# Optimization experiments

Hardware: AMD Instinct MI355X
Metric: run time of the kernel (lower is better)

The kernel has to match this reference:

```python
import jax, jax.numpy as jnp
import numpy as np

N_HEADS = 16
EMBED = 1024
HEAD_SIZE = 64
BLOCK = 2048
BATCH = 2
SEQ = 2048


def setup_inputs() -> dict:
    key = jax.random.key(0)
    ks = jax.random.split(key, 6)
    scale_e = 1.0 / np.sqrt(EMBED)
    x = jax.random.normal(ks[0], (BATCH, SEQ, EMBED), dtype=jnp.float32)
    # per-head Q/K/V projections (bias=False in nanoGPT-style SelfAttentionHead), stacked over heads
    wq = jax.random.normal(ks[1], (N_HEADS, EMBED, HEAD_SIZE), dtype=jnp.float32) * scale_e
    wk = jax.random.normal(ks[2], (N_HEADS, EMBED, HEAD_SIZE), dtype=jnp.float32) * scale_e
    wv = jax.random.normal(ks[3], (N_HEADS, EMBED, HEAD_SIZE), dtype=jnp.float32) * scale_e
    # output projection nn.Linear(embedding_size, embedding_size): y = x @ W^T + b
    w_proj = jax.random.normal(ks[4], (EMBED, EMBED), dtype=jnp.float32) * scale_e
    b_proj = jax.random.normal(ks[5], (EMBED,), dtype=jnp.float32) * 0.01
    return {"x": x, "wq": wq, "wk": wk, "wv": wv, "w_proj": w_proj, "b_proj": b_proj}


def reference(x, wq, wk, wv, w_proj, b_proj):
    B, S, E = x.shape
    # project all heads at once: [B, H, S, D]
    q = jnp.einsum('bse,hed->bhsd', x, wq)
    k = jnp.einsum('bse,hed->bhsd', x, wk)
    v = jnp.einsum('bse,hed->bhsd', x, wv)
    scale = 1.0 / jnp.sqrt(jnp.asarray(HEAD_SIZE, dtype=x.dtype))
    scores = jnp.einsum('bhqd,bhkd->bhqk', q, k) * scale  # [B,H,S,S]
    causal = jnp.tril(jnp.ones((S, S), dtype=bool))
    scores = jnp.where(causal, scores, -jnp.inf)
    attn = jax.nn.softmax(scores, axis=-1)  # (attn dropout inactive in eval)
    out = jnp.einsum('bhqk,bhkd->bhqd', attn, v)  # [B,H,S,D]
    # concat heads along last dim -> [B, S, H*D] == [B, S, E]
    out = out.transpose(0, 2, 1, 3).reshape(B, S, E)
    # output projection (dropout inactive in eval)
    return out @ w_proj.T + b_proj
```

## Files before the change

### kernel.cpp

```cpp
#include <hip/hip_runtime.h>
#include <hip/hip_bf16.h>


typedef __attribute__((ext_vector_type(4))) float  f32x4;
typedef __attribute__((ext_vector_type(8))) short  bf16x8;

#define S_LEN 2048
#define EMB   1024
#define NH    16
#define HD    64

#define LDSW 72

#define QSCALE 0.18033688011112042f
#define EXP2C  17.312340490667562f

#if __has_builtin(__builtin_amdgcn_exp2f)
#define EXP2(x) __builtin_amdgcn_exp2f(x)
#else
#define EXP2(x) __exp2f(x)
#endif

__device__ __forceinline__ unsigned short f2bf(float f) {
    __hip_bfloat16 h = __float2bfloat16(f);
    return __builtin_bit_cast(unsigned short, h);
}
__device__ __forceinline__ unsigned int pk2bf(float a, float b) {
    unsigned int x = __builtin_bit_cast(unsigned int, a);
    unsigned int y = __builtin_bit_cast(unsigned int, b);
    x += 0x7FFFu + ((x >> 16) & 1u);
    y += 0x7FFFu + ((y >> 16) & 1u);
    return (x >> 16) | (y & 0xFFFF0000u);
}

__global__ __launch_bounds__(256) void prep(const float* __restrict__ x,
                                            const float* __restrict__ wq,
                                            const float* __restrict__ wk,
                                            const float* __restrict__ wv,
                                            const float* __restrict__ wproj,
                                            unsigned short* __restrict__ xb,
                                            unsigned short* __restrict__ wpb,
                                            unsigned short* __restrict__ wcat) {
    int blk = blockIdx.x;
    if (blk < 5120) {
        const float* in = (blk < 4096) ? x : wproj;
        unsigned short* out = (blk < 4096) ? xb : wpb;
        int bb = (blk < 4096) ? blk : blk - 4096;
        int i = (bb * 256 + threadIdx.x) * 4;
        float4 v = *(const float4*)(in + i);
        out[i + 0] = f2bf(v.x);
        out[i + 1] = f2bf(v.y);
        out[i + 2] = f2bf(v.z);
        out[i + 3] = f2bf(v.w);
    } else {
        int b2  = blk - 5120;
        int et  = b2 & 7;
        int h   = (b2 >> 3) & 15;
        int qkv = b2 >> 7;
        const float* w = (qkv == 0) ? wq : (qkv == 1) ? wk : wv;
        int t = threadIdx.x;
        int d = t & 63, es = t >> 6;
        int e0 = et * 128 + es * 32;

        unsigned short val[32];
        #pragma unroll
        for (int i = 0; i < 32; i++)
            val[i] = f2bf(w[(size_t)h * 65536 + (size_t)(e0 + i) * 64 + d]);

        size_t n = (size_t)qkv * 1024 + h * 64 + d;
        #pragma unroll
        for (int k = 0; k < 4; k++)
            *(uint4*)(wcat + n * 1024 + e0 + k * 8) = *(const uint4*)(val + k * 8);
    }
}

__device__ __forceinline__ void gemm_tile_core(const unsigned short* __restrict__ A,
                                               const unsigned short* __restrict__ Bt,
                                               int K, int m0, int n0,
                                               unsigned short* As, unsigned short* Bs,
                                               f32x4 acc[4][4]) {
    const int t    = threadIdx.x;
    const int wave = t >> 6, lane = t & 63;
    const int wm   = (wave >> 1) * 64, wn = (wave & 1) * 64;
    const int lr   = lane & 15, quad = lane >> 4;
    const int sr   = t >> 3;
    const int sc   = (t & 7) * 8;

    #pragma unroll
    for (int i = 0; i < 4; i++)
        #pragma unroll
        for (int j = 0; j < 4; j++) acc[i][j] = (f32x4)(0.0f);

    for (int k0 = 0; k0 < K; k0 += 64) {
        __syncthreads();
        #pragma unroll
        for (int p = 0; p < 4; ++p) {
            int r = p * 32 + sr;
            uint4 av = *(const uint4*)(A  + (size_t)(m0 + r) * K + k0 + sc);
            uint4 bv = *(const uint4*)(Bt + (size_t)(n0 + r) * K + k0 + sc);
            *(uint4*)(As + r * LDSW + sc) = av;
            *(uint4*)(Bs + r * LDSW + sc) = bv;
        }
        __syncthreads();
        #pragma unroll
        for (int kk = 0; kk < 64; kk += 32) {
            bf16x8 af[4], bfr[4];
            #pragma unroll
            for (int i = 0; i < 4; i++)
                af[i] = *(const bf16x8*)(As + (wm + i * 16 + lr) * LDSW + kk + quad * 8);
            #pragma unroll
            for (int j = 0; j < 4; j++)
                bfr[j] = *(const bf16x8*)(Bs + (wn + j * 16 + lr) * LDSW + kk + quad * 8);
            #pragma unroll
            for (int i = 0; i < 4; i++)
                #pragma unroll
                for (int j = 0; j < 4; j++)
                    acc[i][j] = __builtin_amdgcn_mfma_f32_16x16x32_bf16(af[i], bfr[j], acc[i][j], 0, 0, 0);
        }
    }
}

__global__ __launch_bounds__(256) void gemm_qkv(const unsigned short* __restrict__ xb,
                                                const unsigned short* __restrict__ wcat,
                                                unsigned short* __restrict__ qb,
                                                unsigned short* __restrict__ kb,
                                                unsigned short* __restrict__ vt) {
    __shared__ unsigned short Smem[2 * 128 * LDSW];
    unsigned short* As = Smem;
    unsigned short* Bs = Smem + 128 * LDSW;
    f32x4 acc[4][4];
    int m0 = blockIdx.x * 128, n0 = blockIdx.y * 128;
    gemm_tile_core(xb, wcat, EMB, m0, n0, As, Bs, acc);

    int t = threadIdx.x, wave = t >> 6, lane = t & 63;
    int wm = (wave >> 1) * 64, wn = (wave & 1) * 64, lr = lane & 15, quad = lane >> 4;
    int b  = m0 >> 11;
    int s0 = m0 & 2047;
    unsigned short* Tb = Smem;

    if (n0 < 2048) {
        bool isQ = (n0 < 1024);
        unsigned short* dst = isQ ? qb : kb;
        float sc = isQ ? QSCALE : 1.0f;
        __syncthreads();
        #pragma unroll
        for (int i = 0; i < 4; i++)
            #pragma unroll
            for (int j = 0; j < 4; j++)
                #pragma unroll
                for (int e = 0; e < 4; e++)
                    Tb[(wm + i * 16 + quad * 4 + e) * 136 + wn + j * 16 + lr] = f2bf(acc[i][j][e] * sc);
        __syncthreads();
        #pragma unroll
        for (int p = 0; p < 8; p++) {
            int r  = p * 16 + (t >> 4);
            int ch = (t & 15) * 8;
            int n  = n0 + ch;
            int h  = (n >> 6) & 15, d = ch & 63;
            *(uint4*)(dst + (((size_t)(b * NH + h)) * S_LEN + s0 + r) * HD + d) =
                *(const uint4*)(Tb + r * 136 + ch);
        }
    } else {
        __syncthreads();
        #pragma unroll
        for (int i = 0; i < 4; i++)
            #pragma unroll
            for (int j = 0; j < 4; j++)
                #pragma unroll
                for (int e = 0; e < 4; e++)
                    Tb[(wn + j * 16 + lr) * 136 + (wm + i * 16 + quad * 4 + e)] = f2bf(acc[i][j][e]);
        __syncthreads();
        #pragma unroll
        for (int p = 0; p < 8; p++) {
            int nl  = p * 16 + (t >> 4);
            int n   = n0 + nl;
            int h   = (n >> 6) & 15, d = n & 63;
            int col = (t & 15) * 8;
            *(uint4*)(vt + (((size_t)(b * NH + h)) * HD + d) * S_LEN + s0 + col) =
                *(const uint4*)(Tb + nl * 136 + col);
        }
    }
}

__global__ __launch_bounds__(256) void gemm_proj(const unsigned short* __restrict__ ao,
                                                 const unsigned short* __restrict__ wpb,
                                                 const float* __restrict__ bproj,
                                                 float* __restrict__ out) {
    __shared__ unsigned short Smem[2 * 128 * LDSW];
    f32x4 acc[4][4];
    int m0 = blockIdx.x * 128, n0 = blockIdx.y * 128;
    gemm_tile_core(ao, wpb, EMB, m0, n0, Smem, Smem + 128 * LDSW, acc);

    int t = threadIdx.x, wave = t >> 6, lane = t & 63;
    int wm = (wave >> 1) * 64, wn = (wave & 1) * 64, lr = lane & 15, quad = lane >> 4;
    #pragma unroll
    for (int i = 0; i < 4; i++)
        #pragma unroll
        for (int j = 0; j < 4; j++) {
            int n = n0 + wn + j * 16 + lr;
            float bias = bproj[n];
            #pragma unroll
            for (int e = 0; e < 4; e++) {
                int m = m0 + wm + i * 16 + quad * 4 + e;
                out[(size_t)m * EMB + n] = acc[i][j][e] + bias;
            }
        }
}

__global__ __launch_bounds__(256) void attn_mfma(const unsigned short* __restrict__ qb,
                                                 const unsigned short* __restrict__ kb,
                                                 const unsigned short* __restrict__ vtb,
                                                 unsigned short* __restrict__ ao) {
    __shared__ unsigned short Ks[64 * LDSW];
    __shared__ unsigned short Vs[64 * LDSW];
    __shared__ unsigned short Ps[64 * LDSW];

    int bIdx = blockIdx.x;
    int bh   = bIdx & 31;
    int sidx = bIdx >> 5;
    int g = sidx >> 3, s = sidx & 7;
    int slab = (g == 0) ? 31 - s : (g == 1) ? s : (g == 2) ? 23 - s : 8 + s;
    int b = bh >> 4, h = bh & 15;
    int t = threadIdx.x, wave = t >> 6, lane = t & 63;
    int c = lane & 15, quad = lane >> 4;

    const unsigned short* Q  = qb  + (size_t)bh * S_LEN * HD;
    const unsigned short* K  = kb  + (size_t)bh * S_LEN * HD;
    const unsigned short* Vt = vtb + (size_t)bh * HD * S_LEN;

    int r0 = slab * 64;
    int rw = r0 + wave * 16;

    bf16x8 Qf[2];
    #pragma unroll
    for (int ks = 0; ks < 2; ks++)
        Qf[ks] = *(const bf16x8*)(Q + (size_t)(rw + c) * HD + ks * 32 + quad * 8);

    f32x4 O[4];
    f32x4 lacc = (f32x4)(0.0f);
    #pragma unroll
    for (int dt = 0; dt < 4; dt++) O[dt] = (f32x4)(0.0f);

    const short oneb = (short)0x3F80;
    bf16x8 ones = {oneb, oneb, oneb, oneb, oneb, oneb, oneb, oneb};

    unsigned short* Pw = Ps + wave * 16 * LDSW;
    int sr = t >> 3, scg = (t & 7) * 8;

    int kend = r0 + 64;
    uint4 kpre0 = *(const uint4*)(K  + (size_t)sr * HD + scg);
    uint4 kpre1 = *(const uint4*)(K  + (size_t)(sr + 32) * HD + scg);
    uint4 vpre0 = *(const uint4*)(Vt + (size_t)sr * S_LEN + scg);
    uint4 vpre1 = *(const uint4*)(Vt + (size_t)(sr + 32) * S_LEN + scg);

    for (int j0 = 0; j0 < kend; j0 += 64) {
        __syncthreads();
        *(uint4*)(Ks + sr * LDSW + scg)        = kpre0;
        *(uint4*)(Ks + (sr + 32) * LDSW + scg) = kpre1;
        *(uint4*)(Vs + sr * LDSW + scg)        = vpre0;
        *(uint4*)(Vs + (sr + 32) * LDSW + scg) = vpre1;
        __syncthreads();
        if (j0 + 64 < kend) {
            kpre0 = *(const uint4*)(K  + (size_t)(j0 + 64 + sr) * HD + scg);
            kpre1 = *(const uint4*)(K  + (size_t)(j0 + 96 + sr) * HD + scg);
            vpre0 = *(const uint4*)(Vt + (size_t)sr * S_LEN + j0 + 64 + scg);
            vpre1 = *(const uint4*)(Vt + (size_t)(sr + 32) * S_LEN + j0 + 64 + scg);
        }

        f32x4 S4[4];
        #pragma unroll
        for (int kt = 0; kt < 4; kt++) S4[kt] = (f32x4)(0.0f);
        __builtin_amdgcn_s_setprio(1);
        #pragma unroll
        for (int ks = 0; ks < 2; ks++) {
            bf16x8 Kf[4];
            #pragma unroll
            for (int kt = 0; kt < 4; kt++)
                Kf[kt] = *(const bf16x8*)(Ks + (kt * 16 + c) * LDSW + ks * 32 + quad * 8);
            #pragma unroll
            for (int kt = 0; kt < 4; kt++)
                S4[kt] = __builtin_amdgcn_mfma_f32_16x16x32_bf16(Kf[kt], Qf[ks], S4[kt], 0, 0, 0);
        }
        __builtin_amdgcn_s_setprio(0);

        bool need_mask = (j0 + 63 > rw);
        #pragma unroll
        for (int kt = 0; kt < 4; kt++) {
            float p0 = EXP2(S4[kt][0] - EXP2C);
            float p1 = EXP2(S4[kt][1] - EXP2C);
            float p2 = EXP2(S4[kt][2] - EXP2C);
            float p3 = EXP2(S4[kt][3] - EXP2C);
            if (need_mask) {
                int key  = j0 + kt * 16 + quad * 4;
                int qrow = rw + c;
                if (key + 0 > qrow) p0 = 0.0f;
                if (key + 1 > qrow) p1 = 0.0f;
                if (key + 2 > qrow) p2 = 0.0f;
                if (key + 3 > qrow) p3 = 0.0f;
            }
            uint2 pk;
            pk.x = pk2bf(p0, p1);
            pk.y = pk2bf(p2, p3);
            *(uint2*)(Pw + c * LDSW + kt * 16 + quad * 4) = pk;
        }

        __builtin_amdgcn_s_setprio(1);
        #pragma unroll
        for (int ks = 0; ks < 2; ks++) {
            bf16x8 Af = *(const bf16x8*)(Pw + c * LDSW + ks * 32 + quad * 8);
            lacc = __builtin_amdgcn_mfma_f32_16x16x32_bf16(Af, ones, lacc, 0, 0, 0);
            #pragma unroll
            for (int dt = 0; dt < 4; dt++) {
                bf16x8 Vf = *(const bf16x8*)(Vs + (dt * 16 + c) * LDSW + ks * 32 + quad * 8);
                O[dt] = __builtin_amdgcn_mfma_f32_16x16x32_bf16(Af, Vf, O[dt], 0, 0, 0);
            }
        }
        __builtin_amdgcn_s_setprio(0);
    }

    float inv[4];
    #pragma unroll
    for (int e = 0; e < 4; e++) inv[e] = 1.0f / lacc[e];

    #pragma unroll
    for (int dt = 0; dt < 4; dt++)
        #pragma unroll
        for (int e = 0; e < 4; e++)
            Ps[(wave * 16 + quad * 4 + e) * LDSW + dt * 16 + c] = f2bf(O[dt][e] * inv[e]);
    __syncthreads();
    #pragma unroll
    for (int p = 0; p < 2; p++) {
        int r = p * 32 + sr;
        *(uint4*)(ao + ((size_t)(b * S_LEN + r0 + r)) * EMB + h * HD + scg) =
            *(const uint4*)(Ps + r * LDSW + scg);
    }
}

extern "C" void kernel_launch(void* const* d_in, const int* in_sizes, int n_in,
                              void* d_out, int out_size, void* d_ws, size_t ws_size,
                              hipStream_t stream) {
    const float* x     = (const float*)d_in[0];
    const float* wq    = (const float*)d_in[1];
    const float* wk    = (const float*)d_in[2];
    const float* wv    = (const float*)d_in[3];
    const float* wproj = (const float*)d_in[4];
    const float* bproj = (const float*)d_in[5];
    float* out = (float*)d_out;

    char* ws = (char*)d_ws;
    unsigned short* xb   = (unsigned short*)(ws + 0);
    unsigned short* wcat = (unsigned short*)(ws + 8388608);
    unsigned short* wpb  = (unsigned short*)(ws + 14680064);
    unsigned short* qb   = (unsigned short*)(ws + 16777216);
    unsigned short* kb   = (unsigned short*)(ws + 25165824);
    unsigned short* vt   = (unsigned short*)(ws + 33554432);
    unsigned short* ao   = (unsigned short*)(ws + 41943040);

    prep<<<5504, 256, 0, stream>>>(x, wq, wk, wv, wproj, xb, wpb, wcat);
    gemm_qkv<<<dim3(32, 24), 256, 0, stream>>>(xb, wcat, qb, kb, vt);
    attn_mfma<<<1024, 256, 0, stream>>>(qb, kb, vt, ao);
    gemm_proj<<<dim3(32, 8), 256, 0, stream>>>(ao, wpb, bproj, out);
}
```

Baseline: 181.2 us.

## Process 128 query rows per attention block with double-buffered K/V tiles

Each attention block now runs 8 waves over a 128-row query chunk, so every K/V tile loaded into LDS serves twice as many query rows. K/V tiles are double-buffered, which cuts the loop to one barrier per tile, and the block order is rebalanced for the causal workload. Waves whose rows lie entirely before a tile skip it, so some waves sit idle at the diagonal. The LDS row pitch drops from 72 to 68, which also changes the GEMM kernels' padding and leaves 16-byte LDS accesses only 8-byte aligned. The fixed exponent offset is removed, which risks overflow in exp2 if scores grow large.

```diff
diff --git a/kernel.cpp b/kernel.cpp
--- a/kernel.cpp
+++ b/kernel.cpp
@@ -10,10 +10,9 @@
 #define NH    16
 #define HD    64
 
-#define LDSW 72
+#define LDSW 68
 
 #define QSCALE 0.18033688011112042f
-#define EXP2C  17.312340490667562f
 
 #if __has_builtin(__builtin_amdgcn_exp2f)
 #define EXP2(x) __builtin_amdgcn_exp2f(x)
@@ -207,19 +206,18 @@
         }
 }
 
-__global__ __launch_bounds__(256) void attn_mfma(const unsigned short* __restrict__ qb,
+__global__ __launch_bounds__(512) void attn_mfma(const unsigned short* __restrict__ qb,
                                                  const unsigned short* __restrict__ kb,
                                                  const unsigned short* __restrict__ vtb,
                                                  unsigned short* __restrict__ ao) {
-    __shared__ unsigned short Ks[64 * LDSW];
-    __shared__ unsigned short Vs[64 * LDSW];
-    __shared__ unsigned short Ps[64 * LDSW];
+    __shared__ unsigned short Ks[2][64 * LDSW];
+    __shared__ unsigned short Vs[2][64 * LDSW];
+    __shared__ unsigned short Ps[128 * LDSW];
 
     int bIdx = blockIdx.x;
     int bh   = bIdx & 31;
-    int sidx = bIdx >> 5;
-    int g = sidx >> 3, s = sidx & 7;
-    int slab = (g == 0) ? 31 - s : (g == 1) ? s : (g == 2) ? 23 - s : 8 + s;
+    int grp  = bIdx >> 5;
+    int chunk = (grp < 8) ? (15 - grp) : (grp - 8);
     int b = bh >> 4, h = bh & 15;
     int t = threadIdx.x, wave = t >> 6, lane = t & 63;
     int c = lane & 15, quad = lane >> 4;
@@ -228,7 +226,7 @@
     const unsigned short* K  = kb  + (size_t)bh * S_LEN * HD;
     const unsigned short* Vt = vtb + (size_t)bh * HD * S_LEN;
 
-    int r0 = slab * 64;
+    int r0 = chunk * 128;
     int rw = r0 + wave * 16;
 
     bf16x8 Qf[2];
@@ -247,75 +245,82 @@
     unsigned short* Pw = Ps + wave * 16 * LDSW;
     int sr = t >> 3, scg = (t & 7) * 8;
 
-    int kend = r0 + 64;
-    uint4 kpre0 = *(const uint4*)(K  + (size_t)sr * HD + scg);
-    uint4 kpre1 = *(const uint4*)(K  + (size_t)(sr + 32) * HD + scg);
-    uint4 vpre0 = *(const uint4*)(Vt + (size_t)sr * S_LEN + scg);
-    uint4 vpre1 = *(const uint4*)(Vt + (size_t)(sr + 32) * S_LEN + scg);
-
-    for (int j0 = 0; j0 < kend; j0 += 64) {
-        __syncthreads();
-        *(uint4*)(Ks + sr * LDSW + scg)        = kpre0;
-        *(uint4*)(Ks + (sr + 32) * LDSW + scg) = kpre1;
-        *(uint4*)(Vs + sr * LDSW + scg)        = vpre0;
-        *(uint4*)(Vs + (sr + 32) * LDSW + scg) = vpre1;
-        __syncthreads();
-        if (j0 + 64 < kend) {
-            kpre0 = *(const uint4*)(K  + (size_t)(j0 + 64 + sr) * HD + scg);
-            kpre1 = *(const uint4*)(K  + (size_t)(j0 + 96 + sr) * HD + scg);
-            vpre0 = *(const uint4*)(Vt + (size_t)sr * S_LEN + j0 + 64 + scg);
-            vpre1 = *(const uint4*)(Vt + (size_t)(sr + 32) * S_LEN + j0 + 64 + scg);
-        }
-
-        f32x4 S4[4];
-        #pragma unroll
-        for (int kt = 0; kt < 4; kt++) S4[kt] = (f32x4)(0.0f);
-        __builtin_amdgcn_s_setprio(1);
-        #pragma unroll
-        for (int ks = 0; ks < 2; ks++) {
-            bf16x8 Kf[4];
-            #pragma unroll
-            for (int kt = 0; kt < 4; kt++)
-                Kf[kt] = *(const bf16x8*)(Ks + (kt * 16 + c) * LDSW + ks * 32 + quad * 8);
-            #pragma unroll
-            for (int kt = 0; kt < 4; kt++)
-                S4[kt] = __builtin_amdgcn_mfma_f32_16x16x32_bf16(Kf[kt], Qf[ks], S4[kt], 0, 0, 0);
-        }
-        __builtin_amdgcn_s_setprio(0);
-
-        bool need_mask = (j0 + 63 > rw);
-        #pragma unroll
-        for (int kt = 0; kt < 4; kt++) {
-            float p0 = EXP2(S4[kt][0] - EXP2C);
-            float p1 = EXP2(S4[kt][1] - EXP2C);
-            float p2 = EXP2(S4[kt][2] - EXP2C);
-            float p3 = EXP2(S4[kt][3] - EXP2C);
-            if (need_mask) {
-                int key  = j0 + kt * 16 + quad * 4;
-                int qrow = rw + c;
-                if (key + 0 > qrow) p0 = 0.0f;
-                if (key + 1 > qrow) p1 = 0.0f;
-                if (key + 2 > qrow) p2 = 0.0f;
-                if (key + 3 > qrow) p3 = 0.0f;
-            }
-            uint2 pk;
-            pk.x = pk2bf(p0, p1);
-            pk.y = pk2bf(p2, p3);
-            *(uint2*)(Pw + c * LDSW + kt * 16 + quad * 4) = pk;
-        }
-
-        __builtin_amdgcn_s_setprio(1);
-        #pragma unroll
-        for (int ks = 0; ks < 2; ks++) {
-            bf16x8 Af = *(const bf16x8*)(Pw + c * LDSW + ks * 32 + quad * 8);
-            lacc = __builtin_amdgcn_mfma_f32_16x16x32_bf16(Af, ones, lacc, 0, 0, 0);
-            #pragma unroll
-            for (int dt = 0; dt < 4; dt++) {
-                bf16x8 Vf = *(const bf16x8*)(Vs + (dt * 16 + c) * LDSW + ks * 32 + quad * 8);
-                O[dt] = __builtin_amdgcn_mfma_f32_16x16x32_bf16(Af, Vf, O[dt], 0, 0, 0);
-            }
-        }
-        __builtin_amdgcn_s_setprio(0);
+    int NT = (r0 + 128) >> 6;
+
+    uint4 kpre = *(const uint4*)(K  + (size_t)sr * HD + scg);
+    uint4 vpre = *(const uint4*)(Vt + (size_t)sr * S_LEN + scg);
+    *(uint4*)(Ks[0] + sr * LDSW + scg) = kpre;
+    *(uint4*)(Vs[0] + sr * LDSW + scg) = vpre;
+    kpre = *(const uint4*)(K  + (size_t)(64 + sr) * HD + scg);
+    vpre = *(const uint4*)(Vt + (size_t)sr * S_LEN + 64 + scg);
+
+    for (int tt = 0; tt < NT; ++tt) {
+        __syncthreads();
+        if (tt + 1 < NT) {
+            unsigned short* Kd = Ks[(tt + 1) & 1];
+            unsigned short* Vd = Vs[(tt + 1) & 1];
+            *(uint4*)(Kd + sr * LDSW + scg) = kpre;
+            *(uint4*)(Vd + sr * LDSW + scg) = vpre;
+            if (tt + 2 < NT) {
+                kpre = *(const uint4*)(K  + (size_t)((tt + 2) * 64 + sr) * HD + scg);
+                vpre = *(const uint4*)(Vt + (size_t)sr * S_LEN + (tt + 2) * 64 + scg);
+            }
+        }
+        int j0 = tt << 6;
+        if (j0 <= rw + 15) {
+            const unsigned short* Kc = Ks[tt & 1];
+            const unsigned short* Vc = Vs[tt & 1];
+
+            f32x4 S4[4];
+            #pragma unroll
+            for (int kt = 0; kt < 4; kt++) S4[kt] = (f32x4)(0.0f);
+            __builtin_amdgcn_s_setprio(1);
+            #pragma unroll
+            for (int ks = 0; ks < 2; ks++) {
+                bf16x8 Kf[4];
+                #pragma unroll
+                for (int kt = 0; kt < 4; kt++)
+                    Kf[kt] = *(const bf16x8*)(Kc + (kt * 16 + c) * LDSW + ks * 32 + quad * 8);
+                #pragma unroll
+                for (int kt = 0; kt < 4; kt++)
+                    S4[kt] = __builtin_amdgcn_mfma_f32_16x16x32_bf16(Kf[kt], Qf[ks], S4[kt], 0, 0, 0);
+            }
+            __builtin_amdgcn_s_setprio(0);
+
+            bool need_mask = (j0 + 63 > rw);
+            #pragma unroll
+            for (int kt = 0; kt < 4; kt++) {
+                float p0 = EXP2(S4[kt][0]);
+                float p1 = EXP2(S4[kt][1]);
+                float p2 = EXP2(S4[kt][2]);
+                float p3 = EXP2(S4[kt][3]);
+                if (need_mask) {
+                    int key  = j0 + kt * 16 + quad * 4;
+                    int qrow = rw + c;
+                    if (key + 0 > qrow) p0 = 0.0f;
+                    if (key + 1 > qrow) p1 = 0.0f;
+                    if (key + 2 > qrow) p2 = 0.0f;
+                    if (key + 3 > qrow) p3 = 0.0f;
+                }
+                uint2 pk;
+                pk.x = pk2bf(p0, p1);
+                pk.y = pk2bf(p2, p3);
+                *(uint2*)(Pw + c * LDSW + kt * 16 + quad * 4) = pk;
+            }
+
+            __builtin_amdgcn_s_setprio(1);
+            #pragma unroll
+            for (int ks = 0; ks < 2; ks++) {
+                bf16x8 Af = *(const bf16x8*)(Pw + c * LDSW + ks * 32 + quad * 8);
+                lacc = __builtin_amdgcn_mfma_f32_16x16x32_bf16(Af, ones, lacc, 0, 0, 0);
+                #pragma unroll
+                for (int dt = 0; dt < 4; dt++) {
+                    bf16x8 Vf = *(const bf16x8*)(Vc + (dt * 16 + c) * LDSW + ks * 32 + quad * 8);
+                    O[dt] = __builtin_amdgcn_mfma_f32_16x16x32_bf16(Af, Vf, O[dt], 0, 0, 0);
+                }
+            }
+            __builtin_amdgcn_s_setprio(0);
+        }
     }
 
     float inv[4];
@@ -330,7 +335,7 @@
     __syncthreads();
     #pragma unroll
     for (int p = 0; p < 2; p++) {
-        int r = p * 32 + sr;
+        int r = p * 64 + sr;
         *(uint4*)(ao + ((size_t)(b * S_LEN + r0 + r)) * EMB + h * HD + scg) =
             *(const uint4*)(Ps + r * LDSW + scg);
     }
@@ -358,6 +363,6 @@
 
     prep<<<5504, 256, 0, stream>>>(x, wq, wk, wv, wproj, xb, wpb, wcat);
     gemm_qkv<<<dim3(32, 24), 256, 0, stream>>>(xb, wcat, qb, kb, vt);
-    attn_mfma<<<1024, 256, 0, stream>>>(qb, kb, vt, ao);
+    attn_mfma<<<512, 512, 0, stream>>>(qb, kb, vt, ao);
     gemm_proj<<<dim3(32, 8), 256, 0, stream>>>(ao, wpb, bproj, out);
 }
```

Measured after the change: 399.5 us. 2.2x slower.
